# Kernel optimization log

Measured on AMD Instinct MI355X. Metric: run time of the kernel, lower is better.

## Reference

```python
import jax, jax.numpy as jnp
import numpy as np
from jax import lax


def setup_inputs() -> dict:
    key = jax.random.key(0)
    k1, k2, k3 = jax.random.split(key, 3)
    X = jax.random.normal(k1, (8192, 8192), dtype=jnp.float32)
    K = jax.random.normal(k2, (7, 7), dtype=jnp.float32)
    bias = jax.random.normal(k3, (1,), dtype=jnp.float32)
    return {"X": X, "K": K, "bias": bias}


def reference(X, K, bias):
    # Valid 2D cross-correlation of X [H, W] with K [kh, kw], plus scalar bias.
    # Output shape: [H - kh + 1, W - kw + 1].
    lhs = X[None, None, :, :]          # NCHW, N=C=1
    rhs = K[None, None, :, :]          # OIHW, O=I=1
    out = lax.conv_general_dilated(
        lhs, rhs,
        window_strides=(1, 1),
        padding='VALID',
        dimension_numbers=('NCHW', 'OIHW', 'NCHW'),
    )
    return out[0, 0] + bias[0]
```

## Files before the change

### kernel.cpp

```cpp
#include <hip/hip_runtime.h>
#include <hip/hip_bf16.h>

#define IN_N   8192
#define OUT_N  8186
#define KS     7

#define WX     112
#define SROW   22
#define NLDW   11
#define LSTR   272
#define WAVE_LDS (SROW * LSTR)
#define NCHUNK 5
#define NPANEL 15
#define NGROUP 128
#define NBLK   (NGROUP * NPANEL)
#define GCHUNK 73

typedef __bf16 bf16x8 __attribute__((ext_vector_type(8)));
typedef float  f32x4  __attribute__((ext_vector_type(4)));

union BFU { __bf16 h; unsigned short u; };
__device__ __forceinline__ unsigned short f2bf(float f) {
    BFU c; c.h = (__bf16)f; return c.u;
}

template<bool G>
struct WavePipe {
    const float* X; float* out;
    char* sb;
    int y0;
    int lo, hi, ls5, l31;
    float bv;
    bf16x8 bfrag[KS];
    float4 ld[NLDW];

    __device__ __forceinline__ void load_chunk(int c) {
        const int xb = c * WX;
        if constexpr (!G) {
            const float* gb = X + (size_t)(y0 + ls5) * IN_N + xb + l31 * 4;
            #pragma unroll
            for (int k = 0; k < NLDW; ++k)
                ld[k] = *(const float4*)(gb + (size_t)(2 * k) * IN_N);
        } else {
            #pragma unroll
            for (int k = 0; k < NLDW; ++k) {
                const int r  = min(y0 + ls5 + 2 * k, IN_N - 1);
                const int cc = min(xb + l31 * 4, IN_N - 4);
                ld[k] = *(const float4*)(X + (size_t)r * IN_N + cc);
            }
        }
    }

    __device__ __forceinline__ void write_chunk() {
        char* lb = sb + ls5 * LSTR + l31 * 8;
        #pragma unroll
        for (int k = 0; k < NLDW; ++k) {
            ushort4 h;
            h.x = f2bf(ld[k].x); h.y = f2bf(ld[k].y);
            h.z = f2bf(ld[k].z); h.w = f2bf(ld[k].w);
            *(ushort4*)(lb + k * 544) = h;
        }
    }

    __device__ __forceinline__ void compute_chunk(int c) {
        const int xb = c * WX;
        const char* ab = sb + lo * LSTR + 16 * hi;
        float* ob = out + (size_t)(y0 + 4 * hi) * OUT_N + xb + lo;
        #pragma unroll
        for (int t8 = 0; t8 < 7; ++t8) {
            f32x4 accA = { bv, bv, bv, bv };
            f32x4 accB = { 0.f, 0.f, 0.f, 0.f };
            bf16x8 a0 = *(const bf16x8*)(ab + 0*LSTR + 32*t8);
            bf16x8 a1 = *(const bf16x8*)(ab + 1*LSTR + 32*t8);
            bf16x8 a2 = *(const bf16x8*)(ab + 2*LSTR + 32*t8);
            bf16x8 a3 = *(const bf16x8*)(ab + 3*LSTR + 32*t8);
            bf16x8 a4 = *(const bf16x8*)(ab + 4*LSTR + 32*t8);
            bf16x8 a5 = *(const bf16x8*)(ab + 5*LSTR + 32*t8);
            bf16x8 a6 = *(const bf16x8*)(ab + 6*LSTR + 32*t8);
            accA = __builtin_amdgcn_mfma_f32_16x16x32_bf16(a0, bfrag[0], accA, 0, 0, 0);
            accB = __builtin_amdgcn_mfma_f32_16x16x32_bf16(a1, bfrag[1], accB, 0, 0, 0);
            accA = __builtin_amdgcn_mfma_f32_16x16x32_bf16(a2, bfrag[2], accA, 0, 0, 0);
            accB = __builtin_amdgcn_mfma_f32_16x16x32_bf16(a3, bfrag[3], accB, 0, 0, 0);
            accA = __builtin_amdgcn_mfma_f32_16x16x32_bf16(a4, bfrag[4], accA, 0, 0, 0);
            accB = __builtin_amdgcn_mfma_f32_16x16x32_bf16(a5, bfrag[5], accB, 0, 0, 0);
            accA = __builtin_amdgcn_mfma_f32_16x16x32_bf16(a6, bfrag[6], accA, 0, 0, 0);
            const f32x4 acc = accA + accB;

            if constexpr (!G) {
                #pragma unroll
                for (int r = 0; r < 4; ++r)
                    ob[(size_t)r * OUT_N + 16 * t8] = acc[r];
            } else {
                const int ox = xb + 16 * t8 + lo;
                if (ox < OUT_N) {
                    #pragma unroll
                    for (int r = 0; r < 4; ++r) {
                        const int oy = y0 + 4 * hi + r;
                        if (oy < OUT_N) ob[(size_t)r * OUT_N + 16 * t8] = acc[r];
                    }
                }
            }
        }
    }

    __device__ __forceinline__ void run(int c0, int nc) {
        load_chunk(c0);
        write_chunk();
        asm volatile("s_waitcnt lgkmcnt(0)" ::: "memory");
        __builtin_amdgcn_sched_barrier(0);

        for (int i = 0; i < nc; ++i) {
            const int c = c0 + i;
            const bool pre = (i + 1 < nc);
            if (pre) load_chunk(c + 1);
            __builtin_amdgcn_sched_barrier(0);
            compute_chunk(c);
            __builtin_amdgcn_sched_barrier(0);
            if (pre) {
                asm volatile("s_waitcnt lgkmcnt(0)" ::: "memory");
                write_chunk();
                asm volatile("s_waitcnt lgkmcnt(0)" ::: "memory");
                __builtin_amdgcn_sched_barrier(0);
            }
        }
    }
};

__global__ __launch_bounds__(256, 4)
void conv7x7_wp(const float* __restrict__ X, const float* __restrict__ Kw,
                const float* __restrict__ bias, float* __restrict__ out) {
    __shared__ __align__(16) char sb_all[4 * WAVE_LDS];

    const int tid  = threadIdx.x;
    const int lane = tid & 63;
    const int wv   = tid >> 6;

    const int bid  = blockIdx.x;
    const int swz  = (bid & 7) * (NBLK / 8) + (bid >> 3);
    const int grp  = swz / NPANEL;
    const int pan  = swz - grp * NPANEL;
    const int band = grp * 4 + wv;

    const int c0 = pan * NCHUNK;
    const int nc = min(NCHUNK, (OUT_N - c0 * WX + WX - 1) / WX);

    WavePipe<false> wp;
    const int lo = lane & 15, hi = lane >> 4;
    bf16x8 bfrag[KS];
    #pragma unroll
    for (int ky = 0; ky < KS; ++ky) {
        bf16x8 bvv;
        #pragma unroll
        for (int e = 0; e < 8; ++e) {
            const int d = 8 * hi + e - lo;
            bvv[e] = (__bf16)((d >= 0 && d < KS) ? Kw[ky * KS + d] : 0.0f);
        }
        bfrag[ky] = bvv;
    }

    const bool guarded = (band == NGROUP * 4 - 1) || (pan == NPANEL - 1);

    if (!guarded) {
        WavePipe<false> p;
        p.X = X; p.out = out; p.sb = sb_all + wv * WAVE_LDS;
        p.y0 = band * 16; p.lo = lo; p.hi = hi;
        p.ls5 = lane >> 5; p.l31 = lane & 31; p.bv = bias[0];
        #pragma unroll
        for (int k = 0; k < KS; ++k) p.bfrag[k] = bfrag[k];
        p.run(c0, nc);
    } else {
        WavePipe<true> p;
        p.X = X; p.out = out; p.sb = sb_all + wv * WAVE_LDS;
        p.y0 = band * 16; p.lo = lo; p.hi = hi;
        p.ls5 = lane >> 5; p.l31 = lane & 31; p.bv = bias[0];
        #pragma unroll
        for (int k = 0; k < KS; ++k) p.bfrag[k] = bfrag[k];
        p.run(c0, nc);
    }
}

extern "C" void kernel_launch(void* const* d_in, const int* in_sizes, int n_in,
                              void* d_out, int out_size, void* d_ws, size_t ws_size,
                              hipStream_t stream) {
    const float* X    = (const float*)d_in[0];
    const float* Kw   = (const float*)d_in[1];
    const float* bias = (const float*)d_in[2];
    float* out = (float*)d_out;

    conv7x7_wp<<<dim3(NBLK), dim3(256), 0, stream>>>(X, Kw, bias, out);
}
```

Baseline: 148.7 us.

## Transpose MFMA operands for row-contiguous stores, rebalance panels, raise compute priority

Swaps the A/B operands of the MFMA so each lane holds four consecutive output columns of one row. The result can then be written as two 8-byte stores instead of four strided scalar stores. Work is split into 12 panels over 74 chunks with a fractional partition, so only the last chunk runs the guarded path. s_setprio is raised around the compute section. The 8-byte stores rely on alignment: OUT_N is even, so rows stay 8-byte aligned, which looks valid.

New measurement: 156.4 us. 1.05x slower.

```diff
diff --git a/kernel.cpp b/kernel.cpp
--- a/kernel.cpp
+++ b/kernel.cpp
@@ -10,11 +10,11 @@
 #define NLDW   11
 #define LSTR   272
 #define WAVE_LDS (SROW * LSTR)
-#define NCHUNK 5
-#define NPANEL 15
+#define NCHT   74
+#define GCH    73
+#define NPANEL 12
 #define NGROUP 128
 #define NBLK   (NGROUP * NPANEL)
-#define GCHUNK 73
 
 typedef __bf16 bf16x8 __attribute__((ext_vector_type(8)));
 typedef float  f32x4  __attribute__((ext_vector_type(4)));
@@ -23,6 +23,7 @@
 __device__ __forceinline__ unsigned short f2bf(float f) {
     BFU c; c.h = (__bf16)f; return c.u;
 }
+union D2 { f32x4 v; double d[2]; };
 
 template<bool G>
 struct WavePipe {
@@ -65,7 +66,8 @@
     __device__ __forceinline__ void compute_chunk(int c) {
         const int xb = c * WX;
         const char* ab = sb + lo * LSTR + 16 * hi;
-        float* ob = out + (size_t)(y0 + 4 * hi) * OUT_N + xb + lo;
+        float* ob = out + (size_t)(y0 + lo) * OUT_N + xb + 4 * hi;
+        __builtin_amdgcn_s_setprio(1);
         #pragma unroll
         for (int t8 = 0; t8 < 7; ++t8) {
             f32x4 accA = { bv, bv, bv, bv };
@@ -77,41 +79,41 @@
             bf16x8 a4 = *(const bf16x8*)(ab + 4*LSTR + 32*t8);
             bf16x8 a5 = *(const bf16x8*)(ab + 5*LSTR + 32*t8);
             bf16x8 a6 = *(const bf16x8*)(ab + 6*LSTR + 32*t8);
-            accA = __builtin_amdgcn_mfma_f32_16x16x32_bf16(a0, bfrag[0], accA, 0, 0, 0);
-            accB = __builtin_amdgcn_mfma_f32_16x16x32_bf16(a1, bfrag[1], accB, 0, 0, 0);
-            accA = __builtin_amdgcn_mfma_f32_16x16x32_bf16(a2, bfrag[2], accA, 0, 0, 0);
-            accB = __builtin_amdgcn_mfma_f32_16x16x32_bf16(a3, bfrag[3], accB, 0, 0, 0);
-            accA = __builtin_amdgcn_mfma_f32_16x16x32_bf16(a4, bfrag[4], accA, 0, 0, 0);
-            accB = __builtin_amdgcn_mfma_f32_16x16x32_bf16(a5, bfrag[5], accB, 0, 0, 0);
-            accA = __builtin_amdgcn_mfma_f32_16x16x32_bf16(a6, bfrag[6], accA, 0, 0, 0);
-            const f32x4 acc = accA + accB;
+            accA = __builtin_amdgcn_mfma_f32_16x16x32_bf16(bfrag[0], a0, accA, 0, 0, 0);
+            accB = __builtin_amdgcn_mfma_f32_16x16x32_bf16(bfrag[1], a1, accB, 0, 0, 0);
+            accA = __builtin_amdgcn_mfma_f32_16x16x32_bf16(bfrag[2], a2, accA, 0, 0, 0);
+            accB = __builtin_amdgcn_mfma_f32_16x16x32_bf16(bfrag[3], a3, accB, 0, 0, 0);
+            accA = __builtin_amdgcn_mfma_f32_16x16x32_bf16(bfrag[4], a4, accA, 0, 0, 0);
+            accB = __builtin_amdgcn_mfma_f32_16x16x32_bf16(bfrag[5], a5, accB, 0, 0, 0);
+            accA = __builtin_amdgcn_mfma_f32_16x16x32_bf16(bfrag[6], a6, accA, 0, 0, 0);
+            D2 acc; acc.v = accA + accB;
 
             if constexpr (!G) {
-                #pragma unroll
-                for (int r = 0; r < 4; ++r)
-                    ob[(size_t)r * OUT_N + 16 * t8] = acc[r];
+                double* po = (double*)(ob + 16 * t8);
+                po[0] = acc.d[0];
+                po[1] = acc.d[1];
             } else {
-                const int ox = xb + 16 * t8 + lo;
-                if (ox < OUT_N) {
+                const int oy = y0 + lo;
+                const int ox = xb + 16 * t8 + 4 * hi;
+                if (oy < OUT_N) {
                     #pragma unroll
-                    for (int r = 0; r < 4; ++r) {
-                        const int oy = y0 + 4 * hi + r;
-                        if (oy < OUT_N) ob[(size_t)r * OUT_N + 16 * t8] = acc[r];
-                    }
+                    for (int r = 0; r < 4; ++r)
+                        if (ox + r < OUT_N) ob[(size_t)16 * t8 + r] = acc.v[r];
                 }
             }
         }
+        __builtin_amdgcn_s_setprio(0);
     }
 
-    __device__ __forceinline__ void run(int c0, int nc) {
+    __device__ __forceinline__ void run(int c0, int c1) {
+        if (c0 >= c1) return;
         load_chunk(c0);
         write_chunk();
         asm volatile("s_waitcnt lgkmcnt(0)" ::: "memory");
         __builtin_amdgcn_sched_barrier(0);
 
-        for (int i = 0; i < nc; ++i) {
-            const int c = c0 + i;
-            const bool pre = (i + 1 < nc);
+        for (int c = c0; c < c1; ++c) {
+            const bool pre = (c + 1 < c1);
             if (pre) load_chunk(c + 1);
             __builtin_amdgcn_sched_barrier(0);
             compute_chunk(c);
@@ -127,8 +129,8 @@
 };
 
 __global__ __launch_bounds__(256, 4)
-void conv7x7_wp(const float* __restrict__ X, const float* __restrict__ Kw,
-                const float* __restrict__ bias, float* __restrict__ out) {
+void conv7x7_t(const float* __restrict__ X, const float* __restrict__ Kw,
+               const float* __restrict__ bias, float* __restrict__ out) {
     __shared__ __align__(16) char sb_all[4 * WAVE_LDS];
 
     const int tid  = threadIdx.x;
@@ -141,10 +143,9 @@
     const int pan  = swz - grp * NPANEL;
     const int band = grp * 4 + wv;
 
-    const int c0 = pan * NCHUNK;
-    const int nc = min(NCHUNK, (OUT_N - c0 * WX + WX - 1) / WX);
+    const int c0 = (NCHT * pan) / NPANEL;
+    const int c1 = (NCHT * (pan + 1)) / NPANEL;
 
-    WavePipe<false> wp;
     const int lo = lane & 15, hi = lane >> 4;
     bf16x8 bfrag[KS];
     #pragma unroll
@@ -158,16 +159,23 @@
         bfrag[ky] = bvv;
     }
 
-    const bool guarded = (band == NGROUP * 4 - 1) || (pan == NPANEL - 1);
-
-    if (!guarded) {
+    if (band < 511) {
         WavePipe<false> p;
         p.X = X; p.out = out; p.sb = sb_all + wv * WAVE_LDS;
         p.y0 = band * 16; p.lo = lo; p.hi = hi;
         p.ls5 = lane >> 5; p.l31 = lane & 31; p.bv = bias[0];
         #pragma unroll
         for (int k = 0; k < KS; ++k) p.bfrag[k] = bfrag[k];
-        p.run(c0, nc);
+        p.run(c0, min(c1, GCH));
+        if (c1 > GCH) {
+            WavePipe<true> q;
+            q.X = X; q.out = out; q.sb = sb_all + wv * WAVE_LDS;
+            q.y0 = band * 16; q.lo = lo; q.hi = hi;
+            q.ls5 = lane >> 5; q.l31 = lane & 31; q.bv = bias[0];
+            #pragma unroll
+            for (int k = 0; k < KS; ++k) q.bfrag[k] = bfrag[k];
+            q.run(GCH, NCHT);
+        }
     } else {
         WavePipe<true> p;
         p.X = X; p.out = out; p.sb = sb_all + wv * WAVE_LDS;
@@ -175,7 +183,7 @@
         p.ls5 = lane >> 5; p.l31 = lane & 31; p.bv = bias[0];
         #pragma unroll
         for (int k = 0; k < KS; ++k) p.bfrag[k] = bfrag[k];
-        p.run(c0, nc);
+        p.run(c0, c1);
     }
 }
 
@@ -187,5 +195,5 @@
     const float* bias = (const float*)d_in[2];
     float* out = (float*)d_out;
 
-    conv7x7_wp<<<dim3(NBLK), dim3(256), 0, stream>>>(X, Kw, bias, out);
+    conv7x7_t<<<dim3(NBLK), dim3(256), 0, stream>>>(X, Kw, bias, out);
 }
```
